# Kernel tuning notes

Measured on AMD Instinct MI355X. Metric: run time of the kernel, lower is better.

## Reference

```python
import jax, jax.numpy as jnp
import numpy as np

HEADS = 64
DIM_HEAD = 64
SCALE = DIM_HEAD ** -0.5
EPS = 1e-6


def setup_inputs() -> dict:
    key = jax.random.key(0)
    ks = jax.random.split(key, 6)
    b, s, dim = 2, 4096, 1024
    inner = HEADS * DIM_HEAD  # 4096
    std = 0.02
    return {
        "x": jax.random.normal(ks[0], (b, s, dim), dtype=jnp.float32),
        "Wq": jax.random.normal(ks[1], (dim, inner), dtype=jnp.float32) * std,
        "Wk": jax.random.normal(ks[2], (dim, inner), dtype=jnp.float32) * std,
        "Wv": jax.random.normal(ks[3], (dim, inner), dtype=jnp.float32) * std,
        "Wo": jax.random.normal(ks[4], (inner, dim), dtype=jnp.float32) * std,
        "bo": jnp.zeros((dim,), dtype=jnp.float32),
    }


def reference(x, Wq, Wk, Wv, Wo, bo):
    b, s, dim = x.shape
    h, dh = HEADS, DIM_HEAD
    # projections -> [b, s, h, dh]
    q = (x @ Wq).reshape(b, s, h, dh)
    k = (x @ Wk).reshape(b, s, h, dh)
    v = (x @ Wv).reshape(b, s, h, dh)
    # kernel feature map (relu) + scale on q
    q = jax.nn.relu(q) * SCALE
    k = jax.nn.relu(k)
    # NOTE: faithful to the source, these einsums contract over the HEAD axis
    # per token (i, j index heads; d indexes dim_head).
    kv = jnp.einsum('bsid,bsjd->bsdj', k, v)          # [b, s, dh, h]
    out = jnp.einsum('bsid,bsdj->bsij', q, kv)        # [b, s, h, h]
    q_norm = jnp.einsum('bsid,bsd->bsi', q, k.sum(axis=2))  # [b, s, h]
    out = out / (q_norm[..., None] + EPS)
    out = out.reshape(b, s, h * h)                    # h*h == h*dh since h == dh
    return out @ Wo + bo
```

## Files before the change

kernel.cpp:

```cpp
#include <hip/hip_runtime.h>
#include <hip/hip_bf16.h>
#include <cstdint>

#define M_TOK 8192
#define DIM   1024
#define INNER 4096
#define HEADS 64
#define DH    64
#define QSCALE 0.125f
#define EPS    1e-6f

typedef __hip_bfloat16 bf16;
typedef __bf16 bf16x8_t __attribute__((ext_vector_type(8)));
typedef float f32x4_t __attribute__((ext_vector_type(4)));

__device__ __forceinline__ float bfbits2f(unsigned short u) {
  return __uint_as_float(((unsigned)u) << 16);
}
__device__ __forceinline__ unsigned short f2bfbits(float f) {
  __hip_bfloat16 h = __float2bfloat16(f);
  unsigned short u;
  __builtin_memcpy(&u, &h, 2);
  return u;
}

__device__ __forceinline__ void load_lds16(const void* g, void* l) {
  __builtin_amdgcn_global_load_lds(
      (__attribute__((address_space(1))) void*)g,
      (__attribute__((address_space(3))) void*)l, 16, 0, 0);
}

__device__ __forceinline__ void swizzle_xy(int& bx, int& by) {
  const int gx = gridDim.x, gy = gridDim.y;
  const int id  = blockIdx.x + gx * blockIdx.y;
  const int per = gy >> 3;
  const int xcd = id & 7;
  const int s   = id >> 3;
  by = xcd * per + (s % per);
  bx = s / per;
}

__global__ __launch_bounds__(256) void castx_kernel(
    const float* __restrict__ x, unsigned short* __restrict__ xb, int n4)
{
  const int i = blockIdx.x * 256 + threadIdx.x;
  if (i < n4) {
    const float4 v = reinterpret_cast<const float4*>(x)[i];
    ushort4 o;
    o.x = f2bfbits(v.x); o.y = f2bfbits(v.y);
    o.z = f2bfbits(v.z); o.w = f2bfbits(v.w);
    reinterpret_cast<ushort4*>(xb)[i] = o;
  }
}

__global__ __launch_bounds__(256) void tcast_kernel(
    const float* __restrict__ W, unsigned short* __restrict__ Wt, int R, int C)
{
  __shared__ float tile[32][33];
  const int bx = blockIdx.x * 32;
  const int by = blockIdx.y * 32;
  const int tx = threadIdx.x & 31;
  const int ty = threadIdx.x >> 5;
#pragma unroll
  for (int k = 0; k < 4; ++k)
    tile[ty + k * 8][tx] = W[(size_t)(by + ty + k * 8) * C + bx + tx];
  __syncthreads();
#pragma unroll
  for (int k = 0; k < 4; ++k)
    Wt[(size_t)(bx + ty + k * 8) * R + by + tx] = f2bfbits(tile[tx][ty + k * 8]);
}

__global__ __launch_bounds__(256) void tcast_dual_kernel(
    const float* __restrict__ W0, const float* __restrict__ W1,
    unsigned short* __restrict__ Wt, int R, int C)
{
  __shared__ float tile[32][33];
  const float* W = blockIdx.z ? W1 : W0;
  unsigned short* dst = Wt + (size_t)blockIdx.z * R * C;
  const int bx = blockIdx.x * 32;
  const int by = blockIdx.y * 32;
  const int tx = threadIdx.x & 31;
  const int ty = threadIdx.x >> 5;
#pragma unroll
  for (int k = 0; k < 4; ++k)
    tile[ty + k * 8][tx] = W[(size_t)(by + ty + k * 8) * C + bx + tx];
  __syncthreads();
#pragma unroll
  for (int k = 0; k < 4; ++k)
    dst[(size_t)(bx + ty + k * 8) * R + by + tx] = f2bfbits(tile[tx][ty + k * 8]);
}

template <int MODE>
__global__ __launch_bounds__(256) void gemm_bf16(
    const unsigned short* __restrict__ A,
    const unsigned short* __restrict__ Bt,
    unsigned short* __restrict__ C,
    int M, int N, int K)
{
  __shared__ __align__(16) unsigned short As[128 * 64];
  __shared__ __align__(16) unsigned short Bs[128 * 64];

  int bxi, byi;
  swizzle_xy(bxi, byi);
  const int tid  = threadIdx.x;
  const int bm   = byi * 128;
  const int bn   = bxi * 128;
  const int lane = tid & 63;
  const int w    = tid >> 6;
  const int wm   = (w & 1) * 64;
  const int wn   = (w >> 1) * 64;
  const int quad = lane >> 4;
  const int l15  = lane & 15;

  f32x4_t acc[4][4];
#pragma unroll
  for (int mt = 0; mt < 4; ++mt)
#pragma unroll
    for (int nt = 0; nt < 4; ++nt) acc[mt][nt] = (f32x4_t){0.f, 0.f, 0.f, 0.f};

  int qa[4], ra[4], ca[4];
#pragma unroll
  for (int j = 0; j < 4; ++j) {
    qa[j] = tid + 256 * j;
    ra[j] = qa[j] >> 3;
    ca[j] = (qa[j] & 7) ^ (ra[j] & 7);
  }

  for (int k0 = 0; k0 < K; k0 += 64) {
    __syncthreads();
#pragma unroll
    for (int j = 0; j < 4; ++j) {
      load_lds16(&A [(size_t)(bm + ra[j]) * K + k0 + ca[j] * 8], &As[qa[j] * 8]);
      load_lds16(&Bt[(size_t)(bn + ra[j]) * K + k0 + ca[j] * 8], &Bs[qa[j] * 8]);
    }
    __syncthreads();

    bf16x8_t af[4][2], bfr[4][2];
#pragma unroll
    for (int mt = 0; mt < 4; ++mt) {
      const int r = wm + mt * 16 + l15;
#pragma unroll
      for (int kt = 0; kt < 2; ++kt) {
        const int slot = (kt * 4 + quad) ^ (r & 7);
        af[mt][kt] = *reinterpret_cast<const bf16x8_t*>(&As[r * 64 + slot * 8]);
      }
    }
#pragma unroll
    for (int nt = 0; nt < 4; ++nt) {
      const int r = wn + nt * 16 + l15;
#pragma unroll
      for (int kt = 0; kt < 2; ++kt) {
        const int slot = (kt * 4 + quad) ^ (r & 7);
        bfr[nt][kt] = *reinterpret_cast<const bf16x8_t*>(&Bs[r * 64 + slot * 8]);
      }
    }
#pragma unroll
    for (int mt = 0; mt < 4; ++mt)
#pragma unroll
      for (int nt = 0; nt < 4; ++nt) {
        acc[mt][nt] = __builtin_amdgcn_mfma_f32_16x16x32_bf16(
            af[mt][0], bfr[nt][0], acc[mt][nt], 0, 0, 0);
        acc[mt][nt] = __builtin_amdgcn_mfma_f32_16x16x32_bf16(
            af[mt][1], bfr[nt][1], acc[mt][nt], 0, 0, 0);
      }
  }

#pragma unroll
  for (int mt = 0; mt < 4; ++mt)
#pragma unroll
    for (int i = 0; i < 4; ++i) {
      const size_t rowg = (size_t)(bm + wm + mt * 16 + quad * 4 + i);
#pragma unroll
      for (int nt = 0; nt < 4; ++nt) {
        float v = acc[mt][nt][i];
        if (MODE >= 1) v = fmaxf(v, 0.f);
        if (MODE == 2) v *= QSCALE;
        C[rowg * N + bn + wn + nt * 16 + l15] = f2bfbits(v);
      }
    }
}

__global__ __launch_bounds__(256) void gemm_kv(
    const unsigned short* __restrict__ A,
    const unsigned short* __restrict__ Bt,
    unsigned short* __restrict__ Kb,
    unsigned short* __restrict__ Vb,
    int K)
{
  __shared__ __align__(16) unsigned short As[128 * 64];
  __shared__ __align__(16) unsigned short Bs[128 * 64];

  int bxi, byi;
  swizzle_xy(bxi, byi);
  const int tid  = threadIdx.x;
  const int bm   = byi * 128;
  const int bn   = bxi * 128;
  const bool isK = (bn < 4096);
  unsigned short* __restrict__ C = isK ? Kb : Vb;
  const int bnc  = bn & 4095;
  const int lane = tid & 63;
  const int w    = tid >> 6;
  const int wm   = (w & 1) * 64;
  const int wn   = (w >> 1) * 64;
  const int quad = lane >> 4;
  const int l15  = lane & 15;

  f32x4_t acc[4][4];
#pragma unroll
  for (int mt = 0; mt < 4; ++mt)
#pragma unroll
    for (int nt = 0; nt < 4; ++nt) acc[mt][nt] = (f32x4_t){0.f, 0.f, 0.f, 0.f};

  int qa[4], ra[4], ca[4];
#pragma unroll
  for (int j = 0; j < 4; ++j) {
    qa[j] = tid + 256 * j;
    ra[j] = qa[j] >> 3;
    ca[j] = (qa[j] & 7) ^ (ra[j] & 7);
  }

  for (int k0 = 0; k0 < K; k0 += 64) {
    __syncthreads();
#pragma unroll
    for (int j = 0; j < 4; ++j) {
      load_lds16(&A [(size_t)(bm + ra[j]) * K + k0 + ca[j] * 8], &As[qa[j] * 8]);
      load_lds16(&Bt[(size_t)(bn + ra[j]) * K + k0 + ca[j] * 8], &Bs[qa[j] * 8]);
    }
    __syncthreads();

    bf16x8_t af[4][2], bfr[4][2];
#pragma unroll
    for (int mt = 0; mt < 4; ++mt) {
      const int r = wm + mt * 16 + l15;
#pragma unroll
      for (int kt = 0; kt < 2; ++kt) {
        const int slot = (kt * 4 + quad) ^ (r & 7);
        af[mt][kt] = *reinterpret_cast<const bf16x8_t*>(&As[r * 64 + slot * 8]);
      }
    }
#pragma unroll
    for (int nt = 0; nt < 4; ++nt) {
      const int r = wn + nt * 16 + l15;
#pragma unroll
      for (int kt = 0; kt < 2; ++kt) {
        const int slot = (kt * 4 + quad) ^ (r & 7);
        bfr[nt][kt] = *reinterpret_cast<const bf16x8_t*>(&Bs[r * 64 + slot * 8]);
      }
    }
#pragma unroll
    for (int mt = 0; mt < 4; ++mt)
#pragma unroll
      for (int nt = 0; nt < 4; ++nt) {
        acc[mt][nt] = __builtin_amdgcn_mfma_f32_16x16x32_bf16(
            af[mt][0], bfr[nt][0], acc[mt][nt], 0, 0, 0);
        acc[mt][nt] = __builtin_amdgcn_mfma_f32_16x16x32_bf16(
            af[mt][1], bfr[nt][1], acc[mt][nt], 0, 0, 0);
      }
  }

#pragma unroll
  for (int mt = 0; mt < 4; ++mt)
#pragma unroll
    for (int i = 0; i < 4; ++i) {
      const size_t rowg = (size_t)(bm + wm + mt * 16 + quad * 4 + i);
#pragma unroll
      for (int nt = 0; nt < 4; ++nt) {
        float v = acc[mt][nt][i];
        if (isK) v = fmaxf(v, 0.f);
        C[rowg * 4096 + bnc + wn + nt * 16 + l15] = f2bfbits(v);
      }
    }
}

__global__ __launch_bounds__(256) void gemm_out_bf16(
    const unsigned short* __restrict__ A,
    const unsigned short* __restrict__ Bt,
    const float* __restrict__ bias,
    float* __restrict__ out, int M, int N, int K)
{
  __shared__ __align__(16) unsigned short As[128 * 64];
  __shared__ __align__(16) unsigned short Bs[64 * 64];

  int bxi, byi;
  swizzle_xy(bxi, byi);
  const int tid  = threadIdx.x;
  const int bm   = byi * 128;
  const int bn   = bxi * 64;
  const int lane = tid & 63;
  const int w    = tid >> 6;
  const int wm   = (w & 1) * 64;
  const int wn   = (w >> 1) * 32;
  const int quad = lane >> 4;
  const int l15  = lane & 15;

  f32x4_t acc[4][2];
#pragma unroll
  for (int mt = 0; mt < 4; ++mt)
#pragma unroll
    for (int nt = 0; nt < 2; ++nt) acc[mt][nt] = (f32x4_t){0.f, 0.f, 0.f, 0.f};

  int qa[4], ra[4], ca[4];
#pragma unroll
  for (int j = 0; j < 4; ++j) {
    qa[j] = tid + 256 * j;
    ra[j] = qa[j] >> 3;
    ca[j] = (qa[j] & 7) ^ (ra[j] & 7);
  }
  int qb[2], rb[2], cb[2];
#pragma unroll
  for (int j = 0; j < 2; ++j) {
    qb[j] = tid + 256 * j;
    rb[j] = qb[j] >> 3;
    cb[j] = (qb[j] & 7) ^ (rb[j] & 7);
  }

  for (int k0 = 0; k0 < K; k0 += 64) {
    __syncthreads();
#pragma unroll
    for (int j = 0; j < 4; ++j)
      load_lds16(&A[(size_t)(bm + ra[j]) * K + k0 + ca[j] * 8], &As[qa[j] * 8]);
#pragma unroll
    for (int j = 0; j < 2; ++j)
      load_lds16(&Bt[(size_t)(bn + rb[j]) * K + k0 + cb[j] * 8], &Bs[qb[j] * 8]);
    __syncthreads();

    bf16x8_t af[4][2], bfr[2][2];
#pragma unroll
    for (int mt = 0; mt < 4; ++mt) {
      const int r = wm + mt * 16 + l15;
#pragma unroll
      for (int kt = 0; kt < 2; ++kt) {
        const int slot = (kt * 4 + quad) ^ (r & 7);
        af[mt][kt] = *reinterpret_cast<const bf16x8_t*>(&As[r * 64 + slot * 8]);
      }
    }
#pragma unroll
    for (int nt = 0; nt < 2; ++nt) {
      const int r = wn + nt * 16 + l15;
#pragma unroll
      for (int kt = 0; kt < 2; ++kt) {
        const int slot = (kt * 4 + quad) ^ (r & 7);
        bfr[nt][kt] = *reinterpret_cast<const bf16x8_t*>(&Bs[r * 64 + slot * 8]);
      }
    }
#pragma unroll
    for (int mt = 0; mt < 4; ++mt)
#pragma unroll
      for (int nt = 0; nt < 2; ++nt) {
        acc[mt][nt] = __builtin_amdgcn_mfma_f32_16x16x32_bf16(
            af[mt][0], bfr[nt][0], acc[mt][nt], 0, 0, 0);
        acc[mt][nt] = __builtin_amdgcn_mfma_f32_16x16x32_bf16(
            af[mt][1], bfr[nt][1], acc[mt][nt], 0, 0, 0);
      }
  }

#pragma unroll
  for (int mt = 0; mt < 4; ++mt)
#pragma unroll
    for (int i = 0; i < 4; ++i) {
      const size_t rowg = (size_t)(bm + wm + mt * 16 + quad * 4 + i);
#pragma unroll
      for (int nt = 0; nt < 2; ++nt) {
        const int colg = bn + wn + nt * 16 + l15;
        out[rowg * N + colg] = acc[mt][nt][i] + bias[colg];
      }
    }
}

__global__ __launch_bounds__(256) void ksum_kernel(
    const unsigned short* __restrict__ Kb, float* __restrict__ ks)
{
  const int t = blockIdx.x * 4 + (threadIdx.x >> 6);
  const int j = threadIdx.x & 63;
  const uint4* row = reinterpret_cast<const uint4*>(Kb + (size_t)t * INNER);
  float s[8] = {0.f, 0.f, 0.f, 0.f, 0.f, 0.f, 0.f, 0.f};
#pragma unroll
  for (int m = 0; m < 8; ++m) {
    const uint4 u = row[j + 64 * m];
    s[0] += __uint_as_float((u.x & 0xFFFFu) << 16);
    s[1] += __uint_as_float(u.x & 0xFFFF0000u);
    s[2] += __uint_as_float((u.y & 0xFFFFu) << 16);
    s[3] += __uint_as_float(u.y & 0xFFFF0000u);
    s[4] += __uint_as_float((u.z & 0xFFFFu) << 16);
    s[5] += __uint_as_float(u.z & 0xFFFF0000u);
    s[6] += __uint_as_float((u.w & 0xFFFFu) << 16);
    s[7] += __uint_as_float(u.w & 0xFFFF0000u);
  }
#pragma unroll
  for (int off = 8; off < 64; off <<= 1)
#pragma unroll
    for (int e = 0; e < 8; ++e) s[e] += __shfl_xor(s[e], off, 64);
  if (j < 8) {
    float4* dst = reinterpret_cast<float4*>(ks + t * 64 + j * 8);
    float4 lo, hi;
    lo.x = s[0]; lo.y = s[1]; lo.z = s[2]; lo.w = s[3];
    hi.x = s[4]; hi.y = s[5]; hi.z = s[6]; hi.w = s[7];
    dst[0] = lo; dst[1] = hi;
  }
}

__global__ __launch_bounds__(256) void attn_mfma(
    const unsigned short* __restrict__ Qb, const unsigned short* __restrict__ Vb,
    const float* __restrict__ ksum, unsigned short* __restrict__ Ab)
{
  const int t    = blockIdx.x * 4 + (threadIdx.x >> 6);
  const int lane = threadIdx.x & 63;
  const int l15  = lane & 15;
  const int quad = lane >> 4;
  const size_t base = (size_t)t * INNER;

  union VU { bf16x8_t v; unsigned short u[8]; };

  float ksv[2][8];
#pragma unroll
  for (int kt = 0; kt < 2; ++kt) {
    const float4* p = reinterpret_cast<const float4*>(ksum + t * 64 + kt * 32 + quad * 8);
    const float4 a = p[0], b = p[1];
    ksv[kt][0] = a.x; ksv[kt][1] = a.y; ksv[kt][2] = a.z; ksv[kt][3] = a.w;
    ksv[kt][4] = b.x; ksv[kt][5] = b.y; ksv[kt][6] = b.z; ksv[kt][7] = b.w;
  }

  bf16x8_t vs[4][2];
#pragma unroll
  for (int nt = 0; nt < 4; ++nt)
#pragma unroll
    for (int kt = 0; kt < 2; ++kt) {
      VU vr, vo;
      vr.v = *reinterpret_cast<const bf16x8_t*>(
          Vb + base + (size_t)(nt * 16 + l15) * 64 + kt * 32 + quad * 8);
#pragma unroll
      for (int j = 0; j < 8; ++j)
        vo.u[j] = f2bfbits(bfbits2f(vr.u[j]) * ksv[kt][j]);
      vs[nt][kt] = vo.v;
    }

  bf16x8_t qf[4][2];
  float qn[4] = {0.f, 0.f, 0.f, 0.f};
#pragma unroll
  for (int mt = 0; mt < 4; ++mt)
#pragma unroll
    for (int kt = 0; kt < 2; ++kt) {
      VU qr;
      qr.v = *reinterpret_cast<const bf16x8_t*>(
          Qb + base + (size_t)(mt * 16 + l15) * 64 + kt * 32 + quad * 8);
      qf[mt][kt] = qr.v;
#pragma unroll
      for (int j = 0; j < 8; ++j)
        qn[mt] += bfbits2f(qr.u[j]) * ksv[kt][j];
    }
#pragma unroll
  for (int mt = 0; mt < 4; ++mt) {
    qn[mt] += __shfl_xor(qn[mt], 16, 64);
    qn[mt] += __shfl_xor(qn[mt], 32, 64);
  }

  f32x4_t acc[4][4];
#pragma unroll
  for (int mt = 0; mt < 4; ++mt)
#pragma unroll
    for (int nt = 0; nt < 4; ++nt) acc[mt][nt] = (f32x4_t){0.f, 0.f, 0.f, 0.f};

#pragma unroll
  for (int mt = 0; mt < 4; ++mt)
#pragma unroll
    for (int nt = 0; nt < 4; ++nt) {
      acc[mt][nt] = __builtin_amdgcn_mfma_f32_16x16x32_bf16(
          qf[mt][0], vs[nt][0], acc[mt][nt], 0, 0, 0);
      acc[mt][nt] = __builtin_amdgcn_mfma_f32_16x16x32_bf16(
          qf[mt][1], vs[nt][1], acc[mt][nt], 0, 0, 0);
    }

#pragma unroll
  for (int mt = 0; mt < 4; ++mt)
#pragma unroll
    for (int i = 0; i < 4; ++i) {
      const float inv = 1.f / (__shfl(qn[mt], quad * 4 + i, 64) + EPS);
      const size_t roff = base + (size_t)(mt * 16 + quad * 4 + i) * 64;
#pragma unroll
      for (int nt = 0; nt < 4; ++nt)
        Ab[roff + nt * 16 + l15] = f2bfbits(acc[mt][nt][i] * inv);
    }
}

extern "C" void kernel_launch(void* const* d_in, const int* in_sizes, int n_in,
                              void* d_out, int out_size, void* d_ws, size_t ws_size,
                              hipStream_t stream)
{
  const float* x  = (const float*)d_in[0];
  const float* Wq = (const float*)d_in[1];
  const float* Wk = (const float*)d_in[2];
  const float* Wv = (const float*)d_in[3];
  const float* Wo = (const float*)d_in[4];
  const float* bo = (const float*)d_in[5];
  float* out = (float*)d_out;

  uint8_t* ws = (uint8_t*)d_ws;
  const size_t HALF = (size_t)M_TOK * INNER * sizeof(bf16);
  unsigned short* KQA = (unsigned short*)ws;
  unsigned short* Vb  = (unsigned short*)(ws + HALF);
  float* ks           = (float*)(ws + 2 * HALF);

  unsigned short* Xb   = (unsigned short*)d_out;
  unsigned short* WtKV = (unsigned short*)((uint8_t*)d_out + (16u << 20));
  unsigned short* WqT  = WtKV;
  unsigned short* Wot  = Vb;

  const dim3 blk(256);

  castx_kernel<<<dim3(M_TOK * DIM / 4 / 256), blk, 0, stream>>>(
      x, Xb, M_TOK * DIM / 4);

  tcast_dual_kernel<<<dim3(INNER / 32, DIM / 32, 2), blk, 0, stream>>>(
      Wk, Wv, WtKV, DIM, INNER);

  gemm_kv<<<dim3(2 * INNER / 128, M_TOK / 128), blk, 0, stream>>>(
      Xb, WtKV, KQA, Vb, DIM);

  ksum_kernel<<<dim3(M_TOK / 4), blk, 0, stream>>>(KQA, ks);

  tcast_kernel<<<dim3(INNER / 32, DIM / 32), blk, 0, stream>>>(
      Wq, WqT, DIM, INNER);

  gemm_bf16<2><<<dim3(INNER / 128, M_TOK / 128), blk, 0, stream>>>(
      Xb, WqT, KQA, M_TOK, INNER, DIM);

  attn_mfma<<<dim3(M_TOK / 4), blk, 0, stream>>>(KQA, Vb, ks, KQA);

  tcast_kernel<<<dim3(DIM / 32, INNER / 32), blk, 0, stream>>>(
      Wo, Wot, INNER, DIM);

  gemm_out_bf16<<<dim3(DIM / 64, M_TOK / 128), blk, 0, stream>>>(
      KQA, Wot, bo, out, M_TOK, DIM, INNER);
}
```

Baseline: 506.7 us.

## Replace projection GEMMs with 256x256 tiled, double-buffered, ping-pong scheduled kernel

Replaces the 128x128 single-buffered projection GEMMs (Q and fused K/V) with a 256x256-tile, 512-thread kernel. It double-buffers B and staggers A loads one tile ahead, interleaving half-tile global-to-LDS staging with MFMA phases under explicit barriers and setprio. The goal is to hide global load latency and raise arithmetic intensity per block. The cost is 128KB of LDS and large register pressure from 32 accumulators, which limits occupancy, and fewer blocks are available for load balance.

Result: faster. 478.0 us (-5.7%).

```diff
diff --git a/kernel.cpp b/kernel.cpp
--- a/kernel.cpp
+++ b/kernel.cpp
@@ -90,186 +90,224 @@
     dst[(size_t)(bx + ty + k * 8) * R + by + tx] = f2bfbits(tile[tx][ty + k * 8]);
 }
 
-template <int MODE>
-__global__ __launch_bounds__(256) void gemm_bf16(
+__device__ __forceinline__ void stage_half(
+    const unsigned short* __restrict__ G, unsigned short* L,
+    int rowbase, int k0, int K, int h, int tid)
+{
+#pragma unroll
+  for (int j = 0; j < 2; ++j) {
+    const int q  = h * 1024 + j * 512 + tid;
+    const int r  = q >> 3;
+    const int cg = (tid & 7) ^ (r & 7);
+    load_lds16(&G[(size_t)(rowbase + r) * K + k0 + cg * 8], &L[q * 8]);
+  }
+}
+
+template <int MODE, int DUAL>
+__global__ __launch_bounds__(512, 2) void gemm256(
     const unsigned short* __restrict__ A,
     const unsigned short* __restrict__ Bt,
-    unsigned short* __restrict__ C,
-    int M, int N, int K)
-{
-  __shared__ __align__(16) unsigned short As[128 * 64];
-  __shared__ __align__(16) unsigned short Bs[128 * 64];
+    unsigned short* __restrict__ C0,
+    unsigned short* __restrict__ C1,
+    int N, int K)
+{
+  __shared__ __align__(16) unsigned short As[2][256 * 64];
+  __shared__ __align__(16) unsigned short Bs[2][256 * 64];
 
   int bxi, byi;
   swizzle_xy(bxi, byi);
   const int tid  = threadIdx.x;
-  const int bm   = byi * 128;
-  const int bn   = bxi * 128;
+  const int bm   = byi * 256;
+  const int bn   = bxi * 256;
   const int lane = tid & 63;
   const int w    = tid >> 6;
-  const int wm   = (w & 1) * 64;
-  const int wn   = (w >> 1) * 64;
+  const int wm   = (w >> 2) * 128;
+  const int wn   = (w & 3) * 64;
   const int quad = lane >> 4;
   const int l15  = lane & 15;
 
-  f32x4_t acc[4][4];
-#pragma unroll
-  for (int mt = 0; mt < 4; ++mt)
+  f32x4_t acc[8][4];
+#pragma unroll
+  for (int mt = 0; mt < 8; ++mt)
 #pragma unroll
     for (int nt = 0; nt < 4; ++nt) acc[mt][nt] = (f32x4_t){0.f, 0.f, 0.f, 0.f};
 
-  int qa[4], ra[4], ca[4];
-#pragma unroll
-  for (int j = 0; j < 4; ++j) {
-    qa[j] = tid + 256 * j;
-    ra[j] = qa[j] >> 3;
-    ca[j] = (qa[j] & 7) ^ (ra[j] & 7);
-  }
-
-  for (int k0 = 0; k0 < K; k0 += 64) {
-    __syncthreads();
-#pragma unroll
-    for (int j = 0; j < 4; ++j) {
-      load_lds16(&A [(size_t)(bm + ra[j]) * K + k0 + ca[j] * 8], &As[qa[j] * 8]);
-      load_lds16(&Bt[(size_t)(bn + ra[j]) * K + k0 + ca[j] * 8], &Bs[qa[j] * 8]);
-    }
-    __syncthreads();
-
-    bf16x8_t af[4][2], bfr[4][2];
+  const int NT = K >> 6;
+
+  stage_half(A,  As[0], bm, 0,  K, 0, tid);
+  stage_half(A,  As[0], bm, 0,  K, 1, tid);
+  stage_half(Bt, Bs[0], bn, 0,  K, 0, tid);
+  stage_half(Bt, Bs[0], bn, 0,  K, 1, tid);
+  stage_half(A,  As[1], bm, 64, K, 0, tid);
+  stage_half(A,  As[1], bm, 64, K, 1, tid);
+  asm volatile("s_waitcnt vmcnt(4)" ::: "memory");
+  __builtin_amdgcn_sched_barrier(0);
+  __builtin_amdgcn_s_barrier();
+  __builtin_amdgcn_sched_barrier(0);
+
+  bf16x8_t af[8][2], bfr[4][2];
+
+  for (int T = 0; T < NT; ++T) {
+    const int c = T & 1;
+    const unsigned short* Ac = As[c];
+    const unsigned short* Bc = Bs[c];
+    unsigned short* Bnx = Bs[c ^ 1];
+    unsigned short* Anx = As[c];
+    const int kB = (T + 1) * 64;
+    const int kA = (T + 2) * 64;
+    const bool pB = (T + 1 < NT);
+    const bool pA = (T + 2 < NT);
+
 #pragma unroll
     for (int mt = 0; mt < 4; ++mt) {
       const int r = wm + mt * 16 + l15;
 #pragma unroll
       for (int kt = 0; kt < 2; ++kt) {
-        const int slot = (kt * 4 + quad) ^ (r & 7);
-        af[mt][kt] = *reinterpret_cast<const bf16x8_t*>(&As[r * 64 + slot * 8]);
-      }
-    }
-#pragma unroll
-    for (int nt = 0; nt < 4; ++nt) {
+        const int s = (kt * 4 + quad) ^ (r & 7);
+        af[mt][kt] = *reinterpret_cast<const bf16x8_t*>(&Ac[r * 64 + s * 8]);
+      }
+    }
+#pragma unroll
+    for (int nt = 0; nt < 2; ++nt) {
       const int r = wn + nt * 16 + l15;
 #pragma unroll
       for (int kt = 0; kt < 2; ++kt) {
-        const int slot = (kt * 4 + quad) ^ (r & 7);
-        bfr[nt][kt] = *reinterpret_cast<const bf16x8_t*>(&Bs[r * 64 + slot * 8]);
-      }
-    }
+        const int s = (kt * 4 + quad) ^ (r & 7);
+        bfr[nt][kt] = *reinterpret_cast<const bf16x8_t*>(&Bc[r * 64 + s * 8]);
+      }
+    }
+    if (pB) stage_half(Bt, Bnx, bn, kB, K, 0, tid);
+    __builtin_amdgcn_sched_barrier(0);
+    __builtin_amdgcn_s_barrier();
+    __builtin_amdgcn_sched_barrier(0);
+    __builtin_amdgcn_s_setprio(1);
 #pragma unroll
     for (int mt = 0; mt < 4; ++mt)
 #pragma unroll
-      for (int nt = 0; nt < 4; ++nt) {
+      for (int nt = 0; nt < 2; ++nt) {
         acc[mt][nt] = __builtin_amdgcn_mfma_f32_16x16x32_bf16(
             af[mt][0], bfr[nt][0], acc[mt][nt], 0, 0, 0);
         acc[mt][nt] = __builtin_amdgcn_mfma_f32_16x16x32_bf16(
             af[mt][1], bfr[nt][1], acc[mt][nt], 0, 0, 0);
       }
-  }
-
-#pragma unroll
-  for (int mt = 0; mt < 4; ++mt)
-#pragma unroll
-    for (int i = 0; i < 4; ++i) {
-      const size_t rowg = (size_t)(bm + wm + mt * 16 + quad * 4 + i);
-#pragma unroll
-      for (int nt = 0; nt < 4; ++nt) {
-        float v = acc[mt][nt][i];
-        if (MODE >= 1) v = fmaxf(v, 0.f);
-        if (MODE == 2) v *= QSCALE;
-        C[rowg * N + bn + wn + nt * 16 + l15] = f2bfbits(v);
-      }
-    }
-}
-
-__global__ __launch_bounds__(256) void gemm_kv(
-    const unsigned short* __restrict__ A,
-    const unsigned short* __restrict__ Bt,
-    unsigned short* __restrict__ Kb,
-    unsigned short* __restrict__ Vb,
-    int K)
-{
-  __shared__ __align__(16) unsigned short As[128 * 64];
-  __shared__ __align__(16) unsigned short Bs[128 * 64];
-
-  int bxi, byi;
-  swizzle_xy(bxi, byi);
-  const int tid  = threadIdx.x;
-  const int bm   = byi * 128;
-  const int bn   = bxi * 128;
-  const bool isK = (bn < 4096);
-  unsigned short* __restrict__ C = isK ? Kb : Vb;
-  const int bnc  = bn & 4095;
-  const int lane = tid & 63;
-  const int w    = tid >> 6;
-  const int wm   = (w & 1) * 64;
-  const int wn   = (w >> 1) * 64;
-  const int quad = lane >> 4;
-  const int l15  = lane & 15;
-
-  f32x4_t acc[4][4];
-#pragma unroll
-  for (int mt = 0; mt < 4; ++mt)
-#pragma unroll
-    for (int nt = 0; nt < 4; ++nt) acc[mt][nt] = (f32x4_t){0.f, 0.f, 0.f, 0.f};
-
-  int qa[4], ra[4], ca[4];
-#pragma unroll
-  for (int j = 0; j < 4; ++j) {
-    qa[j] = tid + 256 * j;
-    ra[j] = qa[j] >> 3;
-    ca[j] = (qa[j] & 7) ^ (ra[j] & 7);
-  }
-
-  for (int k0 = 0; k0 < K; k0 += 64) {
-    __syncthreads();
-#pragma unroll
-    for (int j = 0; j < 4; ++j) {
-      load_lds16(&A [(size_t)(bm + ra[j]) * K + k0 + ca[j] * 8], &As[qa[j] * 8]);
-      load_lds16(&Bt[(size_t)(bn + ra[j]) * K + k0 + ca[j] * 8], &Bs[qa[j] * 8]);
-    }
-    __syncthreads();
-
-    bf16x8_t af[4][2], bfr[4][2];
-#pragma unroll
-    for (int mt = 0; mt < 4; ++mt) {
+    __builtin_amdgcn_s_setprio(0);
+    __builtin_amdgcn_sched_barrier(0);
+    __builtin_amdgcn_s_barrier();
+    __builtin_amdgcn_sched_barrier(0);
+
+#pragma unroll
+    for (int mt = 4; mt < 8; ++mt) {
       const int r = wm + mt * 16 + l15;
 #pragma unroll
       for (int kt = 0; kt < 2; ++kt) {
-        const int slot = (kt * 4 + quad) ^ (r & 7);
-        af[mt][kt] = *reinterpret_cast<const bf16x8_t*>(&As[r * 64 + slot * 8]);
-      }
-    }
-#pragma unroll
-    for (int nt = 0; nt < 4; ++nt) {
+        const int s = (kt * 4 + quad) ^ (r & 7);
+        af[mt][kt] = *reinterpret_cast<const bf16x8_t*>(&Ac[r * 64 + s * 8]);
+      }
+    }
+    if (pB) stage_half(Bt, Bnx, bn, kB, K, 1, tid);
+    __builtin_amdgcn_sched_barrier(0);
+    __builtin_amdgcn_s_barrier();
+    __builtin_amdgcn_sched_barrier(0);
+    __builtin_amdgcn_s_setprio(1);
+#pragma unroll
+    for (int mt = 4; mt < 8; ++mt)
+#pragma unroll
+      for (int nt = 0; nt < 2; ++nt) {
+        acc[mt][nt] = __builtin_amdgcn_mfma_f32_16x16x32_bf16(
+            af[mt][0], bfr[nt][0], acc[mt][nt], 0, 0, 0);
+        acc[mt][nt] = __builtin_amdgcn_mfma_f32_16x16x32_bf16(
+            af[mt][1], bfr[nt][1], acc[mt][nt], 0, 0, 0);
+      }
+    __builtin_amdgcn_s_setprio(0);
+    __builtin_amdgcn_sched_barrier(0);
+    __builtin_amdgcn_s_barrier();
+    __builtin_amdgcn_sched_barrier(0);
+
+#pragma unroll
+    for (int nt = 2; nt < 4; ++nt) {
       const int r = wn + nt * 16 + l15;
 #pragma unroll
       for (int kt = 0; kt < 2; ++kt) {
-        const int slot = (kt * 4 + quad) ^ (r & 7);
-        bfr[nt][kt] = *reinterpret_cast<const bf16x8_t*>(&Bs[r * 64 + slot * 8]);
-      }
-    }
+        const int s = (kt * 4 + quad) ^ (r & 7);
+        bfr[nt][kt] = *reinterpret_cast<const bf16x8_t*>(&Bc[r * 64 + s * 8]);
+      }
+    }
+    if (pA) stage_half(A, Anx, bm, kA, K, 0, tid);
+    __builtin_amdgcn_sched_barrier(0);
+    __builtin_amdgcn_s_barrier();
+    __builtin_amdgcn_sched_barrier(0);
+    __builtin_amdgcn_s_setprio(1);
 #pragma unroll
     for (int mt = 0; mt < 4; ++mt)
 #pragma unroll
-      for (int nt = 0; nt < 4; ++nt) {
+      for (int nt = 2; nt < 4; ++nt) {
         acc[mt][nt] = __builtin_amdgcn_mfma_f32_16x16x32_bf16(
             af[mt][0], bfr[nt][0], acc[mt][nt], 0, 0, 0);
         acc[mt][nt] = __builtin_amdgcn_mfma_f32_16x16x32_bf16(
             af[mt][1], bfr[nt][1], acc[mt][nt], 0, 0, 0);
       }
-  }
-
-#pragma unroll
-  for (int mt = 0; mt < 4; ++mt)
-#pragma unroll
-    for (int i = 0; i < 4; ++i) {
-      const size_t rowg = (size_t)(bm + wm + mt * 16 + quad * 4 + i);
-#pragma unroll
-      for (int nt = 0; nt < 4; ++nt) {
-        float v = acc[mt][nt][i];
-        if (isK) v = fmaxf(v, 0.f);
-        C[rowg * 4096 + bnc + wn + nt * 16 + l15] = f2bfbits(v);
-      }
-    }
+    __builtin_amdgcn_s_setprio(0);
+    __builtin_amdgcn_sched_barrier(0);
+    __builtin_amdgcn_s_barrier();
+    __builtin_amdgcn_sched_barrier(0);
+
+    if (pA) stage_half(A, Anx, bm, kA, K, 1, tid);
+    __builtin_amdgcn_sched_barrier(0);
+    __builtin_amdgcn_s_barrier();
+    __builtin_amdgcn_sched_barrier(0);
+    __builtin_amdgcn_s_setprio(1);
+#pragma unroll
+    for (int mt = 4; mt < 8; ++mt)
+#pragma unroll
+      for (int nt = 2; nt < 4; ++nt) {
+        acc[mt][nt] = __builtin_amdgcn_mfma_f32_16x16x32_bf16(
+            af[mt][0], bfr[nt][0], acc[mt][nt], 0, 0, 0);
+        acc[mt][nt] = __builtin_amdgcn_mfma_f32_16x16x32_bf16(
+            af[mt][1], bfr[nt][1], acc[mt][nt], 0, 0, 0);
+      }
+    __builtin_amdgcn_s_setprio(0);
+    __builtin_amdgcn_sched_barrier(0);
+    if (T < NT - 2) {
+      asm volatile("s_waitcnt vmcnt(4)" ::: "memory");
+    } else {
+      asm volatile("s_waitcnt vmcnt(0)" ::: "memory");
+    }
+    __builtin_amdgcn_sched_barrier(0);
+    __builtin_amdgcn_s_barrier();
+    __builtin_amdgcn_sched_barrier(0);
+  }
+
+  if (DUAL) {
+    const bool isK = (bn < 4096);
+    unsigned short* __restrict__ C = isK ? C0 : C1;
+    const int bnc = bn & 4095;
+#pragma unroll
+    for (int mt = 0; mt < 8; ++mt)
+#pragma unroll
+      for (int i = 0; i < 4; ++i) {
+        const size_t rowg = (size_t)(bm + wm + mt * 16 + quad * 4 + i);
+#pragma unroll
+        for (int nt = 0; nt < 4; ++nt) {
+          float v = acc[mt][nt][i];
+          if (isK) v = fmaxf(v, 0.f);
+          C[rowg * 4096 + bnc + wn + nt * 16 + l15] = f2bfbits(v);
+        }
+      }
+  } else {
+#pragma unroll
+    for (int mt = 0; mt < 8; ++mt)
+#pragma unroll
+      for (int i = 0; i < 4; ++i) {
+        const size_t rowg = (size_t)(bm + wm + mt * 16 + quad * 4 + i);
+#pragma unroll
+        for (int nt = 0; nt < 4; ++nt) {
+          float v = acc[mt][nt][i];
+          if (MODE >= 1) v = fmaxf(v, 0.f);
+          if (MODE == 2) v *= QSCALE;
+          C0[rowg * (size_t)N + bn + wn + nt * 16 + l15] = f2bfbits(v);
+        }
+      }
+  }
 }
 
 __global__ __launch_bounds__(256) void gemm_out_bf16(
@@ -506,6 +544,7 @@
   unsigned short* Wot  = Vb;
 
   const dim3 blk(256);
+  const dim3 blk512(512);
 
   castx_kernel<<<dim3(M_TOK * DIM / 4 / 256), blk, 0, stream>>>(
       x, Xb, M_TOK * DIM / 4);
@@ -513,16 +552,16 @@
   tcast_dual_kernel<<<dim3(INNER / 32, DIM / 32, 2), blk, 0, stream>>>(
       Wk, Wv, WtKV, DIM, INNER);
 
-  gemm_kv<<<dim3(2 * INNER / 128, M_TOK / 128), blk, 0, stream>>>(
-      Xb, WtKV, KQA, Vb, DIM);
+  gemm256<0, 1><<<dim3(2 * INNER / 256, M_TOK / 256), blk512, 0, stream>>>(
+      Xb, WtKV, KQA, Vb, 2 * INNER, DIM);
 
   ksum_kernel<<<dim3(M_TOK / 4), blk, 0, stream>>>(KQA, ks);
 
   tcast_kernel<<<dim3(INNER / 32, DIM / 32), blk, 0, stream>>>(
       Wq, WqT, DIM, INNER);
 
-  gemm_bf16<2><<<dim3(INNER / 128, M_TOK / 128), blk, 0, stream>>>(
-      Xb, WqT, KQA, M_TOK, INNER, DIM);
+  gemm256<2, 0><<<dim3(INNER / 256, M_TOK / 256), blk512, 0, stream>>>(
+      Xb, WqT, KQA, nullptr, INNER, DIM);
 
   attn_mfma<<<dim3(M_TOK / 4), blk, 0, stream>>>(KQA, Vb, ks, KQA);
 
```
